# Optimization experiments

Measured on AMD Instinct MI355X. Metric: run time of the kernel, lower is better.

## Reference

```python
import jax, jax.numpy as jnp
import numpy as np

B, L, D_MODEL, H, D_K, D_V = 64, 52, 4096, 32, 128, 128
NEW_C = D_MODEL // H  # per-head input channel after the (faithful) raw reshape


def setup_inputs() -> dict:
    key = jax.random.key(0)
    ks = jax.random.split(key, 12)
    s = 0.02
    return {
        "Q": jax.random.normal(ks[0], (B, L, D_MODEL), jnp.float32),
        "K": jax.random.normal(ks[1], (B, L, D_MODEL), jnp.float32),
        "V": jax.random.normal(ks[2], (B, L, D_MODEL), jnp.float32),
        "Wq": jax.random.normal(ks[3], (H, NEW_C, D_K), jnp.float32) * s,
        "bq": jnp.zeros((H, D_K), jnp.float32),
        "Wk": jax.random.normal(ks[4], (H, NEW_C, D_K), jnp.float32) * s,
        "bk": jnp.zeros((H, D_K), jnp.float32),
        "Wv": jax.random.normal(ks[5], (H, NEW_C, D_V), jnp.float32) * s,
        "bv": jnp.zeros((H, D_V), jnp.float32),
        "Wo": jax.random.normal(ks[6], (H * D_V, D_MODEL), jnp.float32) * s,
        "bo": jnp.zeros((D_MODEL,), jnp.float32),
    }


def reference(Q, K, V, Wq, bq, Wk, bk, Wv, bv, Wo, bo):
    # Faithful to source: raw reshape (B, L, D) -> (B, H, L, D/H), NOT a channel split.
    def split(x):
        return x.reshape(B, H, L, NEW_C)

    q = jnp.einsum('bhlc,hck->bhlk', split(Q), Wq) + bq[None, :, None, :]  # (B,H,L,D_K)
    k = jnp.einsum('bhlc,hck->bhlk', split(K), Wk) + bk[None, :, None, :]
    v = jnp.einsum('bhlc,hcv->bhlv', split(V), Wv) + bv[None, :, None, :]

    scores = jnp.einsum('bhqk,bhmk->bhqm', q, k) / jnp.sqrt(jnp.asarray(D_K, q.dtype))
    # causal mask: keep j <= i, else -inf (matches the numpy masking loop)
    causal = jnp.tril(jnp.ones((L, L), bool))
    scores = jnp.where(causal[None, None], scores, -jnp.inf)
    attn = jax.nn.softmax(scores, axis=-1)
    o = jnp.einsum('bhqm,bhmv->bhqv', attn, v)  # (B,H,L,D_V)
    o = o.transpose(0, 2, 1, 3).reshape(B, L, H * D_V)  # concat heads on last axis
    # Dropout(0.1) is identity at inference.
    return o @ Wo + bo
```

## Files before the change

kernel.cpp:

```cpp
#include <hip/hip_runtime.h>
#include <hip/hip_bf16.h>

#define B_SZ   64
#define L_SZ   52
#define DMODEL 4096
#define H_SZ   32
#define C_SZ   128
#define DK     128

#define GM 3328
#define GN 4096
#define GK 4096

typedef __bf16 bf16x8 __attribute__((ext_vector_type(8)));
typedef float  f32x4  __attribute__((ext_vector_type(4)));

__device__ __forceinline__ void gload_lds16(const void* g, void* l) {
  __builtin_amdgcn_global_load_lds(
      (__attribute__((address_space(1))) void*)(void*)g,
      (__attribute__((address_space(3))) void*)l, 16, 0, 0);
}

__global__ __launch_bounds__(256) void wo_transpose_kernel(
    const float* __restrict__ Wo, __hip_bfloat16* __restrict__ WoT) {
  __shared__ float tile[64][65];
  const int nt = blockIdx.x, mt = blockIdx.y;
  const int t = threadIdx.x;
  const int r  = t >> 4;
  const int c4 = (t & 15) << 2;
#pragma unroll
  for (int p = 0; p < 4; ++p) {
    const int rr = r + p * 16;
    const float4 v = *(const float4*)(Wo + (size_t)(mt * 64 + rr) * 4096 + nt * 64 + c4);
    tile[rr][c4 + 0] = v.x; tile[rr][c4 + 1] = v.y;
    tile[rr][c4 + 2] = v.z; tile[rr][c4 + 3] = v.w;
  }
  __syncthreads();
#pragma unroll
  for (int p = 0; p < 4; ++p) {
    const int rr = r + p * 16;
    union { __hip_bfloat16 h[4]; ushort4 u; } o4;
#pragma unroll
    for (int e = 0; e < 4; ++e) o4.h[e] = __float2bfloat16(tile[c4 + e][rr]);
    *(ushort4*)(WoT + (size_t)(nt * 64 + rr) * 4096 + mt * 64 + c4) = o4.u;
  }
}

__global__ __launch_bounds__(256) void w3_transpose_kernel(
    const float* __restrict__ Wq, const float* __restrict__ Wk,
    const float* __restrict__ Wv, __hip_bfloat16* __restrict__ WqT,
    __hip_bfloat16* __restrict__ WkT, __hip_bfloat16* __restrict__ WvT) {
  __shared__ float tile[64][65];
  const int bz = blockIdx.z;
  const float* in = (bz < 32 ? Wq : (bz < 64 ? Wk : Wv)) + (size_t)(bz & 31) * 16384;
  __hip_bfloat16* out = (bz < 32 ? WqT : (bz < 64 ? WkT : WvT)) + (size_t)(bz & 31) * 16384;
  const int nt = blockIdx.x, mt = blockIdx.y;
  const int t = threadIdx.x;
  const int r  = t >> 4;
  const int c4 = (t & 15) << 2;
#pragma unroll
  for (int p = 0; p < 4; ++p) {
    const int rr = r + p * 16;
    const float4 v = *(const float4*)(in + (size_t)(mt * 64 + rr) * 128 + nt * 64 + c4);
    tile[rr][c4 + 0] = v.x; tile[rr][c4 + 1] = v.y;
    tile[rr][c4 + 2] = v.z; tile[rr][c4 + 3] = v.w;
  }
  __syncthreads();
#pragma unroll
  for (int p = 0; p < 4; ++p) {
    const int rr = r + p * 16;
    union { __hip_bfloat16 h[4]; ushort4 u; } o4;
#pragma unroll
    for (int e = 0; e < 4; ++e) o4.h[e] = __float2bfloat16(tile[c4 + e][rr]);
    *(ushort4*)(out + (size_t)(nt * 64 + rr) * 128 + mt * 64 + c4) = o4.u;
  }
}

template <bool TRANSPOSED>
__device__ __forceinline__ void wave_proj(
    const __hip_bfloat16* __restrict__ xs, const __hip_bfloat16* __restrict__ WT,
    const float* __restrict__ bias, __hip_bfloat16* __restrict__ out,
    int n0, int r16, int kq) {
  f32x4 acc[4][2] = {};
  bf16x8 bfrag[2][4];
#pragma unroll
  for (int nt = 0; nt < 2; ++nt)
#pragma unroll
    for (int kk = 0; kk < 4; ++kk)
      bfrag[nt][kk] = *(const bf16x8*)(WT + (n0 + nt * 16 + r16) * 128 + kk * 32 + kq * 8);
#pragma unroll
  for (int kk = 0; kk < 4; ++kk) {
    bf16x8 a[4];
#pragma unroll
    for (int mt = 0; mt < 4; ++mt)
      a[mt] = *(const bf16x8*)(xs + (mt * 16 + r16) * 136 + kk * 32 + kq * 8);
#pragma unroll
    for (int mt = 0; mt < 4; ++mt)
#pragma unroll
      for (int nt = 0; nt < 2; ++nt)
        acc[mt][nt] = __builtin_amdgcn_mfma_f32_16x16x32_bf16(a[mt], bfrag[nt][kk], acc[mt][nt], 0, 0, 0);
  }
#pragma unroll
  for (int nt = 0; nt < 2; ++nt) {
    const int col = n0 + nt * 16 + r16;
    const float bv = bias[col];
#pragma unroll
    for (int mt = 0; mt < 4; ++mt) {
      const int m0 = mt * 16 + kq * 4;
      if (!TRANSPOSED) {
#pragma unroll
        for (int i = 0; i < 4; ++i)
          out[(m0 + i) * 136 + col] = __float2bfloat16(acc[mt][nt][i] + bv);
      } else {
        union { __hip_bfloat16 h[4]; ushort4 u; } o4;
        if (m0 < 52) {
#pragma unroll
          for (int i = 0; i < 4; ++i) o4.h[i] = __float2bfloat16(acc[mt][nt][i] + bv);
        } else {
          o4.u = make_ushort4(0, 0, 0, 0);
        }
        *(ushort4*)(out + col * 72 + m0) = o4.u;
      }
    }
  }
}

__global__ __launch_bounds__(256, 2) void attn_kernel(
    const float* __restrict__ Qin, const float* __restrict__ Kin,
    const float* __restrict__ Vin,
    const __hip_bfloat16* __restrict__ WqT, const float* __restrict__ bq,
    const __hip_bfloat16* __restrict__ WkT, const float* __restrict__ bk,
    const __hip_bfloat16* __restrict__ WvT, const float* __restrict__ bv,
    __hip_bfloat16* __restrict__ Oc) {
  __shared__ __align__(16) char lds[70656];
  __hip_bfloat16* xs0  = (__hip_bfloat16*)(lds);
  __hip_bfloat16* xs1  = (__hip_bfloat16*)(lds + 17408);
  __hip_bfloat16* xs2  = (__hip_bfloat16*)(lds + 34816);
  __hip_bfloat16* vT   = (__hip_bfloat16*)(lds + 52224);
  __hip_bfloat16* q_sh = (__hip_bfloat16*)(lds + 34816);
  __hip_bfloat16* k_sh = (__hip_bfloat16*)(lds);
  float*          s_sh = (float*)(lds + 17408);
  __hip_bfloat16* p_sh = (__hip_bfloat16*)(lds + 34816);

  const int h = blockIdx.x, bb = blockIdx.y;
  const int t = threadIdx.x;
  const int w = t >> 6, lane = t & 63;
  const int r16 = lane & 15, kq = lane >> 4;
  const size_t xoff = (size_t)bb * (L_SZ * DMODEL) + (size_t)h * (L_SZ * C_SZ);

  {
    const float* xp[3] = {Qin + xoff, Kin + xoff, Vin + xoff};
    __hip_bfloat16* xd[3] = {xs0, xs1, xs2};
#pragma unroll
    for (int tz = 0; tz < 3; ++tz) {
      const float* X = xp[tz];
      __hip_bfloat16* xs = xd[tz];
      for (int idx = t; idx < 52 * 32; idx += 256) {
        const int row = idx >> 5, c4 = (idx & 31) << 2;
        const float4 v = *(const float4*)(X + row * 128 + c4);
        union { __hip_bfloat16 h[4]; ushort4 u; } o4;
        o4.h[0] = __float2bfloat16(v.x); o4.h[1] = __float2bfloat16(v.y);
        o4.h[2] = __float2bfloat16(v.z); o4.h[3] = __float2bfloat16(v.w);
        *(ushort4*)(xs + row * 136 + c4) = o4.u;
      }
      if (t < 12 * 17) {
        const int row = 52 + t / 17, c8 = (t % 17) * 8;
        *(uint4*)(xs + row * 136 + c8) = make_uint4(0, 0, 0, 0);
      }
    }
  }
  __syncthreads();

  wave_proj<true>(xs2, WvT + (size_t)h * 16384, bv + h * 128, vT, w * 32, r16, kq);
  __syncthreads();
  wave_proj<false>(xs0, WqT + (size_t)h * 16384, bq + h * 128, q_sh, w * 32, r16, kq);
  __syncthreads();
  wave_proj<false>(xs1, WkT + (size_t)h * 16384, bk + h * 128, k_sh, w * 32, r16, kq);
  __syncthreads();

  {
    const int n0 = w * 16;
    f32x4 sacc[4] = {};
#pragma unroll
    for (int kk = 0; kk < 4; ++kk) {
      const bf16x8 bf_ = *(const bf16x8*)(k_sh + (n0 + r16) * 136 + kk * 32 + kq * 8);
#pragma unroll
      for (int mt = 0; mt < 4; ++mt) {
        const bf16x8 a = *(const bf16x8*)(q_sh + (mt * 16 + r16) * 136 + kk * 32 + kq * 8);
        sacc[mt] = __builtin_amdgcn_mfma_f32_16x16x32_bf16(a, bf_, sacc[mt], 0, 0, 0);
      }
    }
    const float scale = 0.08838834764831845f;
#pragma unroll
    for (int mt = 0; mt < 4; ++mt)
#pragma unroll
      for (int i = 0; i < 4; ++i)
        s_sh[(mt * 16 + kq * 4 + i) * 68 + n0 + r16] = sacc[mt][i] * scale;
  }
  __syncthreads();

  {
    const int r = t >> 2, qd = t & 3;
    if (r < 52) {
      float v[16];
      float mx = -3e38f;
#pragma unroll
      for (int j4 = 0; j4 < 4; ++j4) {
        const f32x4 s4 = *(const f32x4*)(s_sh + r * 68 + qd * 16 + j4 * 4);
#pragma unroll
        for (int e = 0; e < 4; ++e) {
          const int col = qd * 16 + j4 * 4 + e;
          const float val = (col <= r) ? s4[e] : -3e38f;
          v[j4 * 4 + e] = val;
          mx = fmaxf(mx, val);
        }
      }
      mx = fmaxf(mx, __shfl_xor(mx, 1));
      mx = fmaxf(mx, __shfl_xor(mx, 2));
      float ex[16];
      float sum = 0.f;
#pragma unroll
      for (int j = 0; j < 16; ++j) {
        const int col = qd * 16 + j;
        const float e = (col <= r) ? __expf(v[j] - mx) : 0.f;
        ex[j] = e; sum += e;
      }
      sum += __shfl_xor(sum, 1);
      sum += __shfl_xor(sum, 2);
      const float inv = 1.0f / sum;
      union { __hip_bfloat16 h[8]; uint4 q; } p0, p1;
#pragma unroll
      for (int j = 0; j < 8; ++j) {
        p0.h[j] = __float2bfloat16(ex[j] * inv);
        p1.h[j] = __float2bfloat16(ex[8 + j] * inv);
      }
      *(uint4*)(p_sh + r * 72 + qd * 16)     = p0.q;
      *(uint4*)(p_sh + r * 72 + qd * 16 + 8) = p1.q;
    } else {
      *(uint4*)(p_sh + r * 72 + qd * 16)     = make_uint4(0, 0, 0, 0);
      *(uint4*)(p_sh + r * 72 + qd * 16 + 8) = make_uint4(0, 0, 0, 0);
    }
  }
  __syncthreads();

  {
    const int n0 = w * 32;
    f32x4 oacc[4][2] = {};
#pragma unroll
    for (int kk = 0; kk < 2; ++kk) {
      bf16x8 bfr[2];
#pragma unroll
      for (int nt = 0; nt < 2; ++nt)
        bfr[nt] = *(const bf16x8*)(vT + (n0 + nt * 16 + r16) * 72 + kk * 32 + kq * 8);
#pragma unroll
      for (int mt = 0; mt < 4; ++mt) {
        const bf16x8 a = *(const bf16x8*)(p_sh + (mt * 16 + r16) * 72 + kk * 32 + kq * 8);
#pragma unroll
        for (int nt = 0; nt < 2; ++nt)
          oacc[mt][nt] = __builtin_amdgcn_mfma_f32_16x16x32_bf16(a, bfr[nt], oacc[mt][nt], 0, 0, 0);
      }
    }
    const size_t obase = (size_t)bb * 52 * 4096 + (size_t)h * 128;
#pragma unroll
    for (int nt = 0; nt < 2; ++nt) {
      const int col = n0 + nt * 16 + r16;
#pragma unroll
      for (int mt = 0; mt < 4; ++mt) {
        const int row0 = mt * 16 + kq * 4;
#pragma unroll
        for (int i = 0; i < 4; ++i) {
          const int row = row0 + i;
          if (row < 52)
            Oc[obase + (size_t)row * 4096 + col] = __float2bfloat16(oacc[mt][nt][i]);
        }
      }
    }
  }
}

#define STAGE(GBASE, REGOFF, KT, KS, WB) do {                                  \
    const __hip_bfloat16* s_ = (GBASE) + (size_t)(KT) * 64 + (KS) * 32;        \
    char* d_ = (WB) + (REGOFF) + ((KS) ? 16384 : 0) + t * 16;                  \
    gload_lds16(s_, d_);                                                       \
    gload_lds16(s_ + (size_t)128 * GK, d_ + 8192);                             \
  } while (0)

#define MFMA16(MQ, BF)                                                         \
  __builtin_amdgcn_sched_barrier(0);                                           \
  __builtin_amdgcn_s_setprio(1);                                               \
  _Pragma("unroll")                                                            \
  for (int mf = 0; mf < 4; ++mf)                                               \
    _Pragma("unroll")                                                          \
    for (int nf = 0; nf < 4; ++nf)                                             \
      acc[(MQ) * 4 + mf][nf] = __builtin_amdgcn_mfma_f32_16x16x32_bf16(        \
          af[mf], BF[nf], acc[(MQ) * 4 + mf][nf], 0, 0, 0);                    \
  __builtin_amdgcn_s_setprio(0)

#define READ_AF(KS, MQ)                                                        \
  _Pragma("unroll")                                                            \
  for (int mf = 0; mf < 4; ++mf)                                               \
    af[mf] = *(const bf16x8*)(rb + (KS) * 16384 + (MQ) * 4096 + aB0 + mf * 1024)

#define READ_BF(BF, KS)                                                        \
  _Pragma("unroll")                                                            \
  for (int nf = 0; nf < 4; ++nf)                                               \
    BF[nf] = *(const bf16x8*)(rb + 32768 + (KS) * 16384 + bB0 + nf * 1024)

__global__ __launch_bounds__(512, 2) void out_gemm_kernel(
    const __hip_bfloat16* __restrict__ A, const __hip_bfloat16* __restrict__ Bt,
    const float* __restrict__ bias, float* __restrict__ C) {
  __shared__ __align__(16) char lds[131072];

  int bid = blockIdx.x;
  bid = (bid & 7) * 26 + (bid >> 3);
  const int tm = bid >> 4;
  const int tn = bid & 15;

  const int t = threadIdx.x;
  const int w = t >> 6, lane = t & 63;
  const int wm = w >> 2, wn = w & 3;
  const int r16 = lane & 15, kq = lane >> 4;

  const int srow = t >> 2;
  const int sgslot = (t & 3) ^ ((srow >> 1) & 3);
  const __hip_bfloat16* gA0 = A  + (size_t)(tm * 256 + srow) * GK + sgslot * 8;
  const __hip_bfloat16* gB0 = Bt + (size_t)(tn * 256 + srow) * GK + sgslot * 8;

  const int slotr = kq ^ ((r16 >> 1) & 3);
  const int aB0 = (wm * 128 + r16) * 64 + slotr * 16;
  const int bB0 = (wn * 64 + r16) * 64 + slotr * 16;

  f32x4 acc[8][4] = {};
  bf16x8 bf0[4], bf1[4];

  STAGE(gA0, 0,     0, 0, lds);
  STAGE(gA0, 0,     0, 1, lds);
  STAGE(gB0, 32768, 0, 0, lds);
  STAGE(gB0, 32768, 0, 1, lds);
  STAGE(gB0, 32768, 1, 0, lds + 65536);
  STAGE(gA0, 0,     1, 0, lds + 65536);
  STAGE(gB0, 32768, 1, 1, lds + 65536);
  asm volatile("s_waitcnt vmcnt(6)" ::: "memory");
  __builtin_amdgcn_s_barrier();

#pragma unroll 1
  for (int kt = 0; kt < 64; ++kt) {
    char* rb = lds + ((kt & 1) << 16);
    char* ob = lds + (((kt + 1) & 1) << 16);
    const int s1 = kt + 1 < 64 ? kt + 1 : 63;
    const int s2 = kt + 2 < 64 ? kt + 2 : 63;

    {
      bf16x8 af[4];
      READ_AF(0, 0);
      READ_BF(bf0, 0);
      STAGE(gA0, 0, s1, 1, ob);
      __builtin_amdgcn_s_barrier();
      asm volatile("s_waitcnt lgkmcnt(0)" ::: "memory");
      MFMA16(0, bf0);
      __builtin_amdgcn_s_barrier();
    }
    {
      bf16x8 af[4];
      READ_AF(0, 1);
      STAGE(gB0, 32768, s2, 0, rb);
      __builtin_amdgcn_s_barrier();
      asm volatile("s_waitcnt lgkmcnt(0)" ::: "memory");
      MFMA16(1, bf0);
      __builtin_amdgcn_s_barrier();
    }
    {
      bf16x8 af[4];
      READ_AF(1, 0);
      READ_BF(bf1, 1);
      STAGE(gA0, 0, s2, 0, rb);
      __builtin_amdgcn_s_barrier();
      asm volatile("s_waitcnt lgkmcnt(0)" ::: "memory");
      MFMA16(0, bf1);
      __builtin_amdgcn_s_barrier();
    }
    {
      bf16x8 af[4];
      READ_AF(1, 1);
      STAGE(gB0, 32768, s2, 1, rb);
      __builtin_amdgcn_s_barrier();
      asm volatile("s_waitcnt lgkmcnt(0)" ::: "memory");
      MFMA16(1, bf1);
      asm volatile("s_waitcnt vmcnt(6)" ::: "memory");
      __builtin_amdgcn_s_barrier();
    }
  }
  asm volatile("s_waitcnt vmcnt(0) lgkmcnt(0)" ::: "memory");

  const int row0 = tm * 256 + wm * 128 + kq * 4;
  const int col0 = tn * 256 + wn * 64 + r16;
#pragma unroll
  for (int nf = 0; nf < 4; ++nf) {
    const int col = col0 + nf * 16;
    const float bv = bias[col];
#pragma unroll
    for (int mf = 0; mf < 8; ++mf) {
      const int row = row0 + mf * 16;
#pragma unroll
      for (int i = 0; i < 4; ++i)
        C[(size_t)(row + i) * GN + col] = acc[mf][nf][i] + bv;
    }
  }
}

extern "C" void kernel_launch(void* const* d_in, const int* in_sizes, int n_in,
                              void* d_out, int out_size, void* d_ws, size_t ws_size,
                              hipStream_t stream) {
  const float* Q  = (const float*)d_in[0];
  const float* K  = (const float*)d_in[1];
  const float* V  = (const float*)d_in[2];
  const float* Wq = (const float*)d_in[3];
  const float* bq = (const float*)d_in[4];
  const float* Wk = (const float*)d_in[5];
  const float* bk = (const float*)d_in[6];
  const float* Wv = (const float*)d_in[7];
  const float* bv = (const float*)d_in[8];
  const float* Wo = (const float*)d_in[9];
  const float* bo = (const float*)d_in[10];
  float* out = (float*)d_out;

  char* wsb = (char*)d_ws;
  __hip_bfloat16* WoT = (__hip_bfloat16*)wsb;
  __hip_bfloat16* Oc  = (__hip_bfloat16*)(wsb + (size_t)GN * GK * 2);
  __hip_bfloat16* WqT = (__hip_bfloat16*)(wsb + (size_t)GN * GK * 2 + (size_t)GM * GN * 2);
  __hip_bfloat16* WkT = WqT + (size_t)H_SZ * C_SZ * DK;
  __hip_bfloat16* WvT = WkT + (size_t)H_SZ * C_SZ * DK;

  w3_transpose_kernel<<<dim3(2, 2, 96), 256, 0, stream>>>(Wq, Wk, Wv, WqT, WkT, WvT);
  wo_transpose_kernel<<<dim3(64, 64), 256, 0, stream>>>(Wo, WoT);
  attn_kernel<<<dim3(H_SZ, B_SZ), 256, 0, stream>>>(Q, K, V, WqT, bq, WkT, bk, WvT, bv, Oc);
  out_gemm_kernel<<<dim3(13 * 16), 512, 0, stream>>>(Oc, WoT, bo, out);
}
```

Baseline: 216.7 us.

## Load projection inputs directly from global memory instead of staging through LDS

The Q/K/V projection now reads fp32 activations straight from global memory into MFMA A-fragments and converts them to bf16 in registers, replacing the LDS staging pass. The LDS layout is reorganised so the q, k and vT buffers no longer alias each other, which removes three of the four barriers around the projections. Each of the four waves now reloads every input row for its own column slice, so global/L2 traffic per block grows about fourfold. Padding rows are clamped to row 51 rather than zero-filled, which affects only rows that are later masked or ignored.

```diff
diff --git a/kernel.cpp b/kernel.cpp
--- a/kernel.cpp
+++ b/kernel.cpp
@@ -77,8 +77,8 @@
 }
 
 template <bool TRANSPOSED>
-__device__ __forceinline__ void wave_proj(
-    const __hip_bfloat16* __restrict__ xs, const __hip_bfloat16* __restrict__ WT,
+__device__ __forceinline__ void proj_g(
+    const float* __restrict__ X, const __hip_bfloat16* __restrict__ WT,
     const float* __restrict__ bias, __hip_bfloat16* __restrict__ out,
     int n0, int r16, int kq) {
   f32x4 acc[4][2] = {};
@@ -92,8 +92,18 @@
   for (int kk = 0; kk < 4; ++kk) {
     bf16x8 a[4];
 #pragma unroll
-    for (int mt = 0; mt < 4; ++mt)
-      a[mt] = *(const bf16x8*)(xs + (mt * 16 + r16) * 136 + kk * 32 + kq * 8);
+    for (int mt = 0; mt < 4; ++mt) {
+      const int row = mt * 16 + r16;
+      const int rowc = row < 52 ? row : 51;
+      const float4* xp = (const float4*)(X + rowc * 128 + kk * 32 + kq * 8);
+      const float4 x0 = xp[0], x1 = xp[1];
+      union { __hip_bfloat16 h[8]; bf16x8 v; } cv;
+      cv.h[0] = __float2bfloat16(x0.x); cv.h[1] = __float2bfloat16(x0.y);
+      cv.h[2] = __float2bfloat16(x0.z); cv.h[3] = __float2bfloat16(x0.w);
+      cv.h[4] = __float2bfloat16(x1.x); cv.h[5] = __float2bfloat16(x1.y);
+      cv.h[6] = __float2bfloat16(x1.z); cv.h[7] = __float2bfloat16(x1.w);
+      a[mt] = cv.v;
+    }
 #pragma unroll
     for (int mt = 0; mt < 4; ++mt)
 #pragma unroll
@@ -133,57 +143,30 @@
     const __hip_bfloat16* __restrict__ WvT, const float* __restrict__ bv,
     __hip_bfloat16* __restrict__ Oc) {
   __shared__ __align__(16) char lds[70656];
-  __hip_bfloat16* xs0  = (__hip_bfloat16*)(lds);
-  __hip_bfloat16* xs1  = (__hip_bfloat16*)(lds + 17408);
-  __hip_bfloat16* xs2  = (__hip_bfloat16*)(lds + 34816);
-  __hip_bfloat16* vT   = (__hip_bfloat16*)(lds + 52224);
-  __hip_bfloat16* q_sh = (__hip_bfloat16*)(lds + 34816);
-  __hip_bfloat16* k_sh = (__hip_bfloat16*)(lds);
-  float*          s_sh = (float*)(lds + 17408);
-  __hip_bfloat16* p_sh = (__hip_bfloat16*)(lds + 34816);
+  __hip_bfloat16* q_sh = (__hip_bfloat16*)(lds);
+  __hip_bfloat16* k_sh = (__hip_bfloat16*)(lds + 17408);
+  __hip_bfloat16* vT   = (__hip_bfloat16*)(lds + 34816);
+  float*          s_sh = (float*)(lds + 53248);
+  __hip_bfloat16* p_sh = (__hip_bfloat16*)(lds);
 
   const int h = blockIdx.x, bb = blockIdx.y;
   const int t = threadIdx.x;
   const int w = t >> 6, lane = t & 63;
   const int r16 = lane & 15, kq = lane >> 4;
   const size_t xoff = (size_t)bb * (L_SZ * DMODEL) + (size_t)h * (L_SZ * C_SZ);
+  const int n0 = w * 32;
+
+  proj_g<false>(Qin + xoff, WqT + (size_t)h * 16384, bq + h * 128, q_sh, n0, r16, kq);
+  proj_g<false>(Kin + xoff, WkT + (size_t)h * 16384, bk + h * 128, k_sh, n0, r16, kq);
+  proj_g<true >(Vin + xoff, WvT + (size_t)h * 16384, bv + h * 128, vT,   n0, r16, kq);
+  __syncthreads();
 
   {
-    const float* xp[3] = {Qin + xoff, Kin + xoff, Vin + xoff};
-    __hip_bfloat16* xd[3] = {xs0, xs1, xs2};
-#pragma unroll
-    for (int tz = 0; tz < 3; ++tz) {
-      const float* X = xp[tz];
-      __hip_bfloat16* xs = xd[tz];
-      for (int idx = t; idx < 52 * 32; idx += 256) {
-        const int row = idx >> 5, c4 = (idx & 31) << 2;
-        const float4 v = *(const float4*)(X + row * 128 + c4);
-        union { __hip_bfloat16 h[4]; ushort4 u; } o4;
-        o4.h[0] = __float2bfloat16(v.x); o4.h[1] = __float2bfloat16(v.y);
-        o4.h[2] = __float2bfloat16(v.z); o4.h[3] = __float2bfloat16(v.w);
-        *(ushort4*)(xs + row * 136 + c4) = o4.u;
-      }
-      if (t < 12 * 17) {
-        const int row = 52 + t / 17, c8 = (t % 17) * 8;
-        *(uint4*)(xs + row * 136 + c8) = make_uint4(0, 0, 0, 0);
-      }
-    }
-  }
-  __syncthreads();
-
-  wave_proj<true>(xs2, WvT + (size_t)h * 16384, bv + h * 128, vT, w * 32, r16, kq);
-  __syncthreads();
-  wave_proj<false>(xs0, WqT + (size_t)h * 16384, bq + h * 128, q_sh, w * 32, r16, kq);
-  __syncthreads();
-  wave_proj<false>(xs1, WkT + (size_t)h * 16384, bk + h * 128, k_sh, w * 32, r16, kq);
-  __syncthreads();
-
-  {
-    const int n0 = w * 16;
+    const int nq = w * 16;
     f32x4 sacc[4] = {};
 #pragma unroll
     for (int kk = 0; kk < 4; ++kk) {
-      const bf16x8 bf_ = *(const bf16x8*)(k_sh + (n0 + r16) * 136 + kk * 32 + kq * 8);
+      const bf16x8 bf_ = *(const bf16x8*)(k_sh + (nq + r16) * 136 + kk * 32 + kq * 8);
 #pragma unroll
       for (int mt = 0; mt < 4; ++mt) {
         const bf16x8 a = *(const bf16x8*)(q_sh + (mt * 16 + r16) * 136 + kk * 32 + kq * 8);
@@ -195,7 +178,7 @@
     for (int mt = 0; mt < 4; ++mt)
 #pragma unroll
       for (int i = 0; i < 4; ++i)
-        s_sh[(mt * 16 + kq * 4 + i) * 68 + n0 + r16] = sacc[mt][i] * scale;
+        s_sh[(mt * 16 + kq * 4 + i) * 68 + nq + r16] = sacc[mt][i] * scale;
   }
   __syncthreads();
 
@@ -244,7 +227,6 @@
   __syncthreads();
 
   {
-    const int n0 = w * 32;
     f32x4 oacc[4][2] = {};
 #pragma unroll
     for (int kk = 0; kk < 2; ++kk) {
```

New measurement: 237.4 us. +9.6%, slower.

## Keep V projection in registers and shrink LDS to fit three blocks per CU

Applied to the files above, without the earlier changes.

The V projection result now stays in registers and is rearranged with cross-lane shuffles into the B-operand layout for the P·V MFMA, so the transposed V tile in LDS is gone. LDS is cut from about 70KB to about 42KB by dropping the zero-padded rows and clamping out-of-range row reads to row 51. Launch bounds rise to 3 blocks per CU to raise occupancy. The trade-off is extra shuffle instructions, higher register pressure, and reliance on the clamped padding rows being masked out of the results.

```diff
diff --git a/kernel.cpp b/kernel.cpp
--- a/kernel.cpp
+++ b/kernel.cpp
@@ -19,6 +19,12 @@
   __builtin_amdgcn_global_load_lds(
       (__attribute__((address_space(1))) void*)(void*)g,
       (__attribute__((address_space(3))) void*)l, 16, 0, 0);
+}
+
+__device__ __forceinline__ unsigned short bfbits(float x) {
+  union { __hip_bfloat16 h; unsigned short u; } c;
+  c.h = __float2bfloat16(x);
+  return c.u;
 }
 
 __global__ __launch_bounds__(256) void wo_transpose_kernel(
@@ -76,8 +82,7 @@
   }
 }
 
-template <bool TRANSPOSED>
-__device__ __forceinline__ void wave_proj(
+__device__ __forceinline__ void proj_lds(
     const __hip_bfloat16* __restrict__ xs, const __hip_bfloat16* __restrict__ WT,
     const float* __restrict__ bias, __hip_bfloat16* __restrict__ out,
     int n0, int r16, int kq) {
@@ -92,8 +97,11 @@
   for (int kk = 0; kk < 4; ++kk) {
     bf16x8 a[4];
 #pragma unroll
-    for (int mt = 0; mt < 4; ++mt)
-      a[mt] = *(const bf16x8*)(xs + (mt * 16 + r16) * 136 + kk * 32 + kq * 8);
+    for (int mt = 0; mt < 4; ++mt) {
+      const int row = mt * 16 + r16;
+      const int rowc = row < 52 ? row : 51;
+      a[mt] = *(const bf16x8*)(xs + rowc * 136 + kk * 32 + kq * 8);
+    }
 #pragma unroll
     for (int mt = 0; mt < 4; ++mt)
 #pragma unroll
@@ -107,50 +115,47 @@
 #pragma unroll
     for (int mt = 0; mt < 4; ++mt) {
       const int m0 = mt * 16 + kq * 4;
-      if (!TRANSPOSED) {
+      if (m0 < 52) {
 #pragma unroll
         for (int i = 0; i < 4; ++i)
-          out[(m0 + i) * 136 + col] = __float2bfloat16(acc[mt][nt][i] + bv);
-      } else {
-        union { __hip_bfloat16 h[4]; ushort4 u; } o4;
-        if (m0 < 52) {
-#pragma unroll
-          for (int i = 0; i < 4; ++i) o4.h[i] = __float2bfloat16(acc[mt][nt][i] + bv);
-        } else {
-          o4.u = make_ushort4(0, 0, 0, 0);
-        }
-        *(ushort4*)(out + col * 72 + m0) = o4.u;
-      }
-    }
-  }
-}
-
-__global__ __launch_bounds__(256, 2) void attn_kernel(
+          if (m0 + i < 52)
+            out[(m0 + i) * 136 + col] = __float2bfloat16(acc[mt][nt][i] + bv);
+      }
+    }
+  }
+}
+
+__device__ __forceinline__ uint2 shfl64(uint2 v, int lane) {
+  uint2 r;
+  r.x = (unsigned)__shfl((int)v.x, lane);
+  r.y = (unsigned)__shfl((int)v.y, lane);
+  return r;
+}
+
+__global__ __launch_bounds__(256, 3) void attn_kernel(
     const float* __restrict__ Qin, const float* __restrict__ Kin,
     const float* __restrict__ Vin,
     const __hip_bfloat16* __restrict__ WqT, const float* __restrict__ bq,
     const __hip_bfloat16* __restrict__ WkT, const float* __restrict__ bk,
     const __hip_bfloat16* __restrict__ WvT, const float* __restrict__ bv,
     __hip_bfloat16* __restrict__ Oc) {
-  __shared__ __align__(16) char lds[70656];
-  __hip_bfloat16* xs0  = (__hip_bfloat16*)(lds);
-  __hip_bfloat16* xs1  = (__hip_bfloat16*)(lds + 17408);
-  __hip_bfloat16* xs2  = (__hip_bfloat16*)(lds + 34816);
-  __hip_bfloat16* vT   = (__hip_bfloat16*)(lds + 52224);
-  __hip_bfloat16* q_sh = (__hip_bfloat16*)(lds + 34816);
-  __hip_bfloat16* k_sh = (__hip_bfloat16*)(lds);
-  float*          s_sh = (float*)(lds + 17408);
-  __hip_bfloat16* p_sh = (__hip_bfloat16*)(lds + 34816);
+  __shared__ __align__(16) char lds[42432];
+  __hip_bfloat16* r0 = (__hip_bfloat16*)(lds);
+  __hip_bfloat16* r1 = (__hip_bfloat16*)(lds + 14144);
+  __hip_bfloat16* r2 = (__hip_bfloat16*)(lds + 28288);
+  float*          s_sh = (float*)(lds + 14144);
+  __hip_bfloat16* p_sh = r0;
 
   const int h = blockIdx.x, bb = blockIdx.y;
   const int t = threadIdx.x;
   const int w = t >> 6, lane = t & 63;
   const int r16 = lane & 15, kq = lane >> 4;
   const size_t xoff = (size_t)bb * (L_SZ * DMODEL) + (size_t)h * (L_SZ * C_SZ);
+  const int n0 = w * 32;
 
   {
     const float* xp[3] = {Qin + xoff, Kin + xoff, Vin + xoff};
-    __hip_bfloat16* xd[3] = {xs0, xs1, xs2};
+    __hip_bfloat16* xd[3] = {r0, r1, r2};
 #pragma unroll
     for (int tz = 0; tz < 3; ++tz) {
       const float* X = xp[tz];
@@ -163,30 +168,68 @@
         o4.h[2] = __float2bfloat16(v.z); o4.h[3] = __float2bfloat16(v.w);
         *(ushort4*)(xs + row * 136 + c4) = o4.u;
       }
-      if (t < 12 * 17) {
-        const int row = 52 + t / 17, c8 = (t % 17) * 8;
-        *(uint4*)(xs + row * 136 + c8) = make_uint4(0, 0, 0, 0);
-      }
-    }
-  }
-  __syncthreads();
-
-  wave_proj<true>(xs2, WvT + (size_t)h * 16384, bv + h * 128, vT, w * 32, r16, kq);
-  __syncthreads();
-  wave_proj<false>(xs0, WqT + (size_t)h * 16384, bq + h * 128, q_sh, w * 32, r16, kq);
-  __syncthreads();
-  wave_proj<false>(xs1, WkT + (size_t)h * 16384, bk + h * 128, k_sh, w * 32, r16, kq);
-  __syncthreads();
-
+    }
+  }
+  __syncthreads();
+
+  uint2 vb[4][2];
   {
-    const int n0 = w * 16;
+    f32x4 acc[4][2] = {};
+    bf16x8 bfrag[2][4];
+    const __hip_bfloat16* WT = WvT + (size_t)h * 16384;
+#pragma unroll
+    for (int nt = 0; nt < 2; ++nt)
+#pragma unroll
+      for (int kk = 0; kk < 4; ++kk)
+        bfrag[nt][kk] = *(const bf16x8*)(WT + (n0 + nt * 16 + r16) * 128 + kk * 32 + kq * 8);
+#pragma unroll
+    for (int kk = 0; kk < 4; ++kk) {
+      bf16x8 a[4];
+#pragma unroll
+      for (int mt = 0; mt < 4; ++mt) {
+        const int row = mt * 16 + r16;
+        const int rowc = row < 52 ? row : 51;
+        a[mt] = *(const bf16x8*)(r2 + rowc * 136 + kk * 32 + kq * 8);
+      }
+#pragma unroll
+      for (int mt = 0; mt < 4; ++mt)
+#pragma unroll
+        for (int nt = 0; nt < 2; ++nt)
+          acc[mt][nt] = __builtin_amdgcn_mfma_f32_16x16x32_bf16(a[mt], bfrag[nt][kk], acc[mt][nt], 0, 0, 0);
+    }
+#pragma unroll
+    for (int nt = 0; nt < 2; ++nt) {
+      const float bvv = bv[h * 128 + n0 + nt * 16 + r16];
+#pragma unroll
+      for (int mt = 0; mt < 4; ++mt) {
+        vb[mt][nt].x = (unsigned)bfbits(acc[mt][nt][0] + bvv) |
+                       ((unsigned)bfbits(acc[mt][nt][1] + bvv) << 16);
+        vb[mt][nt].y = (unsigned)bfbits(acc[mt][nt][2] + bvv) |
+                       ((unsigned)bfbits(acc[mt][nt][3] + bvv) << 16);
+      }
+    }
+  }
+  __syncthreads();
+
+  proj_lds(r0, WqT + (size_t)h * 16384, bq + h * 128, r2, n0, r16, kq);
+  __syncthreads();
+
+  proj_lds(r1, WkT + (size_t)h * 16384, bk + h * 128, r0, n0, r16, kq);
+  __syncthreads();
+
+  {
+    const int nq = w * 16;
     f32x4 sacc[4] = {};
 #pragma unroll
     for (int kk = 0; kk < 4; ++kk) {
-      const bf16x8 bf_ = *(const bf16x8*)(k_sh + (n0 + r16) * 136 + kk * 32 + kq * 8);
+      const int krow = nq + r16;
+      const int krc = krow < 52 ? krow : 51;
+      const bf16x8 bf_ = *(const bf16x8*)(r0 + krc * 136 + kk * 32 + kq * 8);
 #pragma unroll
       for (int mt = 0; mt < 4; ++mt) {
-        const bf16x8 a = *(const bf16x8*)(q_sh + (mt * 16 + r16) * 136 + kk * 32 + kq * 8);
+        const int qrow = mt * 16 + r16;
+        const int qrc = qrow < 52 ? qrow : 51;
+        const bf16x8 a = *(const bf16x8*)(r2 + qrc * 136 + kk * 32 + kq * 8);
         sacc[mt] = __builtin_amdgcn_mfma_f32_16x16x32_bf16(a, bf_, sacc[mt], 0, 0, 0);
       }
     }
@@ -194,8 +237,10 @@
 #pragma unroll
     for (int mt = 0; mt < 4; ++mt)
 #pragma unroll
-      for (int i = 0; i < 4; ++i)
-        s_sh[(mt * 16 + kq * 4 + i) * 68 + n0 + r16] = sacc[mt][i] * scale;
+      for (int i = 0; i < 4; ++i) {
+        const int row = mt * 16 + kq * 4 + i;
+        if (row < 52) s_sh[row * 68 + nq + r16] = sacc[mt][i] * scale;
+      }
   }
   __syncthreads();
 
@@ -236,25 +281,36 @@
       }
       *(uint4*)(p_sh + r * 72 + qd * 16)     = p0.q;
       *(uint4*)(p_sh + r * 72 + qd * 16 + 8) = p1.q;
-    } else {
-      *(uint4*)(p_sh + r * 72 + qd * 16)     = make_uint4(0, 0, 0, 0);
-      *(uint4*)(p_sh + r * 72 + qd * 16 + 8) = make_uint4(0, 0, 0, 0);
     }
   }
   __syncthreads();
 
   {
-    const int n0 = w * 32;
+    const int half = (kq >> 1) & 1;
+    const int src0 = ((kq & 1) << 5) + r16;
+    const int src1 = src0 + 16;
     f32x4 oacc[4][2] = {};
 #pragma unroll
     for (int kk = 0; kk < 2; ++kk) {
       bf16x8 bfr[2];
 #pragma unroll
-      for (int nt = 0; nt < 2; ++nt)
-        bfr[nt] = *(const bf16x8*)(vT + (n0 + nt * 16 + r16) * 72 + kk * 32 + kq * 8);
+      for (int nt = 0; nt < 2; ++nt) {
+        const uint2 a0 = shfl64(vb[2 * kk + 0][nt], src0);
+        const uint2 a1 = shfl64(vb[2 * kk + 1][nt], src0);
+        const uint2 b0 = shfl64(vb[2 * kk + 0][nt], src1);
+        const uint2 b1 = shfl64(vb[2 * kk + 1][nt], src1);
+        union { unsigned u[4]; bf16x8 v; } asm_;
+        asm_.u[0] = half ? a1.x : a0.x;
+        asm_.u[1] = half ? a1.y : a0.y;
+        asm_.u[2] = half ? b1.x : b0.x;
+        asm_.u[3] = half ? b1.y : b0.y;
+        bfr[nt] = asm_.v;
+      }
 #pragma unroll
       for (int mt = 0; mt < 4; ++mt) {
-        const bf16x8 a = *(const bf16x8*)(p_sh + (mt * 16 + r16) * 72 + kk * 32 + kq * 8);
+        const int prow = mt * 16 + r16;
+        const int prc = prow < 52 ? prow : 51;
+        const bf16x8 a = *(const bf16x8*)(p_sh + prc * 72 + kk * 32 + kq * 8);
 #pragma unroll
         for (int nt = 0; nt < 2; ++nt)
           oacc[mt][nt] = __builtin_amdgcn_mfma_f32_16x16x32_bf16(a, bfr[nt], oacc[mt][nt], 0, 0, 0);
```

Result: faster. 207.3 us (-4.3%).
